# Kernel optimization log

Hardware: AMD Instinct MI355X
Metric: run time of the kernel (lower is better)

## Reference

```python
import jax, jax.numpy as jnp
import numpy as np

N = 50000   # nodes
E = 800000  # edges (avg degree 16)
D = 64      # input_nf = output_nf = hidden_nf


def lrelu(x):
    # nn.LeakyReLU(0.2)
    return jnp.where(x >= 0, x, 0.2 * x)


def setup_inputs() -> dict:
    key = jax.random.key(0)
    ks = jax.random.split(key, 12)
    def lin(k, fan_in, fan_out):
        s = 1.0 / np.sqrt(fan_in)
        return jax.random.uniform(k, (fan_in, fan_out), jnp.float32, -s, s)
    inp = {
        "h": jax.random.normal(ks[0], (N, D), jnp.float32),
        "coord": jax.random.normal(ks[1], (N, 3), jnp.float32),
        "edge_index": jax.random.randint(ks[2], (2, E), 0, N, jnp.int32),
        # edge_mlp: Linear(2D+1, D) -> lrelu -> Linear(D, D) -> lrelu
        "w1e": lin(ks[3], 2 * D + 1, D), "b1e": jnp.zeros((D,), jnp.float32),
        "w2e": lin(ks[4], D, D),         "b2e": jnp.zeros((D,), jnp.float32),
        # node_mlp: Linear(2D, D) -> lrelu -> Linear(D, D)
        "w1n": lin(ks[5], 2 * D, D),     "b1n": jnp.zeros((D,), jnp.float32),
        "w2n": lin(ks[6], D, D),         "b2n": jnp.zeros((D,), jnp.float32),
    }
    return inp


def reference(h, coord, edge_index, w1e, b1e, w2e, b2e, w1n, b1n, w2n, b2n):
    row, col = edge_index[0], edge_index[1]
    # coord2radial
    coord_diff = coord[row] - coord[col]                    # [E, 3]
    radial = jnp.sum(coord_diff ** 2, axis=1, keepdims=True)  # [E, 1]
    # edge_model: concat(h[row], h[col], radial) -> MLP
    e_in = jnp.concatenate([h[row], h[col], radial], axis=1)  # [E, 2D+1]
    e = lrelu(e_in @ w1e + b1e)
    edge_feat = lrelu(e @ w2e + b2e)                        # [E, D]
    # node_model: unsorted_segment_sum over row, then MLP, residual
    agg = jax.ops.segment_sum(edge_feat, row, num_segments=N)  # [N, D]
    n_in = jnp.concatenate([h, agg], axis=1)                # [N, 2D]
    out = lrelu(n_in @ w1n + b1n) @ w2n + b2n               # [N, D]
    h_out = h + out                                         # residual=True
    # coords_weight == 0.0 -> coord passes through unchanged
    return (h_out, coord, edge_feat)
```

## Files before the change

kernel.cpp:

```cpp
#include <hip/hip_runtime.h>

#define NN 50000
#define NE 800000
#define D 64
#define SCAN_B 1024
#define NB ((NN + SCAN_B - 1) / SCAN_B)
#define TILES 5
#define EPB (64 * TILES)

typedef __attribute__((ext_vector_type(8))) short bf16x8;
typedef __attribute__((ext_vector_type(4))) float f32x4;
typedef __attribute__((ext_vector_type(4))) unsigned int u32x4;

__device__ __forceinline__ float lrelu(float x) { return x >= 0.0f ? x : 0.2f * x; }

__device__ __forceinline__ unsigned short f2bf(float f) {
    unsigned int x = __float_as_uint(f);
    unsigned int r = (x + 0x7fffu + ((x >> 16) & 1u)) >> 16;
    return (unsigned short)r;
}

__device__ __forceinline__ void wave_lds_fence() {
    asm volatile("s_waitcnt lgkmcnt(0)" ::: "memory");
    __builtin_amdgcn_sched_barrier(0);
}

__global__ __launch_bounds__(256) void prep_count(const float* __restrict__ h,
                                                  unsigned short* __restrict__ hb,
                                                  const int* __restrict__ ei,
                                                  int* __restrict__ counts,
                                                  const float* __restrict__ w1e,
                                                  const float* __restrict__ w2e,
                                                  const float* __restrict__ w1n,
                                                  const float* __restrict__ w2n,
                                                  unsigned short* __restrict__ w1t,
                                                  unsigned short* __restrict__ w2t,
                                                  unsigned short* __restrict__ w1nt,
                                                  unsigned short* __restrict__ w2nt)
{
    int i = blockIdx.x * 256 + threadIdx.x;
    float4 v = ((const float4*)h)[i];
    ushort4 o;
    o.x = f2bf(v.x); o.y = f2bf(v.y); o.z = f2bf(v.z); o.w = f2bf(v.w);
    ((ushort4*)hb)[i] = o;
    atomicAdd(&counts[ei[i]], 1);
    if (i < 8192) {
        int j = i >> 7, k = i & 127;
        w1t[i] = f2bf(w1e[k * 64 + j]);
    } else if (i < 12288) {
        int t2 = i - 8192;
        int j = t2 >> 6, k = t2 & 63;
        w2t[t2] = f2bf(w2e[k * 64 + j]);
    } else if (i < 20480) {
        int t3 = i - 12288;
        int j = t3 >> 7, k = t3 & 127;
        w1nt[t3] = f2bf(w1n[k * 64 + j]);
    } else if (i < 24576) {
        int t4 = i - 20480;
        int j = t4 >> 6, k = t4 & 63;
        w2nt[t4] = f2bf(w2n[k * 64 + j]);
    }
}

__global__ __launch_bounds__(SCAN_B) void scan_block_kernel(const int* __restrict__ counts,
                                                            int* __restrict__ offs,
                                                            int* __restrict__ bsums)
{
    int i = blockIdx.x * SCAN_B + threadIdx.x;
    int v = (i < NN) ? counts[i] : 0;
    int lane = threadIdx.x & 63;
    int wid = threadIdx.x >> 6;
    int x = v;
#pragma unroll
    for (int d = 1; d < 64; d <<= 1) {
        int y = __shfl_up(x, d);
        if (lane >= d) x += y;
    }
    __shared__ int wsum[16];
    if (lane == 63) wsum[wid] = x;
    __syncthreads();
    if (wid == 0) {
        int s = (lane < 16) ? wsum[lane] : 0;
#pragma unroll
        for (int d = 1; d < 16; d <<= 1) {
            int y = __shfl_up(s, d);
            if (lane >= d) s += y;
        }
        if (lane < 16) wsum[lane] = s;
    }
    __syncthreads();
    int woff = (wid == 0) ? 0 : wsum[wid - 1];
    int excl = woff + x - v;
    if (i < NN) offs[i] = excl;
    if (threadIdx.x == 0) bsums[blockIdx.x] = wsum[15];
}

__global__ void scan_top_kernel(int* __restrict__ bsums)
{
    if (threadIdx.x == 0 && blockIdx.x == 0) {
        int run = 0;
        for (int b = 0; b < NB; b++) { int t = bsums[b]; bsums[b] = run; run += t; }
    }
}

__global__ __launch_bounds__(SCAN_B) void add_back_kernel(int* __restrict__ offs,
                                                          const int* __restrict__ bsums,
                                                          int* __restrict__ cursor)
{
    int i = blockIdx.x * SCAN_B + threadIdx.x;
    if (i < NN) {
        int o = offs[i] + bsums[blockIdx.x];
        offs[i] = o;
        cursor[i] = o;
    }
}

__global__ __launch_bounds__(256) void scatter_kernel(const int* __restrict__ ei,
                                                      int* __restrict__ cursor,
                                                      int* __restrict__ csr,
                                                      int* __restrict__ rowpos,
                                                      int* __restrict__ colv)
{
    int e = blockIdx.x * 256 + threadIdx.x;
    if (e < NE) {
        int r = ei[e];
        int pos = atomicAdd(&cursor[r], 1);
        csr[pos] = e;
        rowpos[pos] = r;
        colv[pos] = ei[NE + e];
    }
}

__global__ __launch_bounds__(256) void egnn_edge_mfma(
    const unsigned short* __restrict__ hb, const float* __restrict__ coord,
    const int* __restrict__ csr, const int* __restrict__ rowpos,
    const int* __restrict__ colv,
    const unsigned short* __restrict__ w1t, const float* __restrict__ b1e,
    const float* __restrict__ w1e,
    const unsigned short* __restrict__ w2t, const float* __restrict__ b2e,
    float* __restrict__ edge_feat, float* __restrict__ agg)
{
    __shared__ unsigned short W1[64 * 128];
    __shared__ unsigned short W2[64 * 64];
    __shared__ unsigned short Mb[4][16 * 64];
    __shared__ float Ob[4][16 * 64];

    const int t = threadIdx.x;
    const int orig = blockIdx.x;
    const int xcd = orig & 7, idx8 = orig >> 3;
    const int blk = (xcd < 4 ? xcd * 313 : 4 * 313 + (xcd - 4) * 312) + idx8;

    const int lane = t & 63, wv = t >> 6;
    const int lo = lane & 15, hi = lane >> 4;

    for (int c = t; c < 1024; c += 256) {
        int j = c >> 4, ci = c & 15;
        uint4 v = *(const uint4*)(w1t + j * 128 + ci * 8);
        *(uint4*)((char*)W1 + ((j * 256 + ci * 16) ^ ((j & 7) << 4))) = v;
    }
    for (int c = t; c < 512; c += 256) {
        int j = c >> 3, ci = c & 7;
        uint4 v = *(const uint4*)(w2t + j * 64 + ci * 8);
        *(uint4*)((char*)W2 + ((j * 128 + ci * 16) ^ ((j & 7) << 4))) = v;
    }
    float bj1[4], wl1[4], bj2[4];
#pragma unroll
    for (int ct = 0; ct < 4; ct++) {
        bj1[ct] = b1e[ct * 16 + lo];
        wl1[ct] = w1e[128 * 64 + ct * 16 + lo];
        bj2[ct] = b2e[ct * 16 + lo];
    }
    __syncthreads();

    char* w1b = (char*)W1;
    char* w2b = (char*)W2;
    char* mb = (char*)Mb[wv];
    char* ob = (char*)Ob[wv];

    const int pbase = blk * EPB + wv * (16 * TILES);

    int e5[TILES], row5[TILES], col5[TILES];
    float rad5[TILES];
#pragma unroll
    for (int tl = 0; tl < TILES; tl++) {
        int p = pbase + tl * 16 + lo;
        e5[tl] = csr[p];
        row5[tl] = rowpos[p];
        col5[tl] = colv[p];
    }
#pragma unroll
    for (int tl = 0; tl < TILES; tl++) {
        float dx = coord[row5[tl] * 3 + 0] - coord[col5[tl] * 3 + 0];
        float dy = coord[row5[tl] * 3 + 1] - coord[col5[tl] * 3 + 1];
        float dz = coord[row5[tl] * 3 + 2] - coord[col5[tl] * 3 + 2];
        rad5[tl] = dx * dx + dy * dy + dz * dz;
    }

    uint4 aR0, aR1, aC0, aC1, nR0, nR1, nC0, nC1;
    aR0 = *(const uint4*)(hb + (size_t)row5[0] * 64 + hi * 8);
    aR1 = *(const uint4*)(hb + (size_t)row5[0] * 64 + 32 + hi * 8);
    aC0 = *(const uint4*)(hb + (size_t)col5[0] * 64 + hi * 8);
    aC1 = *(const uint4*)(hb + (size_t)col5[0] * 64 + 32 + hi * 8);

#pragma unroll
    for (int tl = 0; tl < TILES; tl++) {
        if (tl + 1 < TILES) {
            nR0 = *(const uint4*)(hb + (size_t)row5[tl + 1] * 64 + hi * 8);
            nR1 = *(const uint4*)(hb + (size_t)row5[tl + 1] * 64 + 32 + hi * 8);
            nC0 = *(const uint4*)(hb + (size_t)col5[tl + 1] * 64 + hi * 8);
            nC1 = *(const uint4*)(hb + (size_t)col5[tl + 1] * 64 + 32 + hi * 8);
        }

        float radr[4];
#pragma unroll
        for (int r = 0; r < 4; r++) radr[r] = __shfl(rad5[tl], hi * 4 + r);
        f32x4 acc[4];
#pragma unroll
        for (int ct = 0; ct < 4; ct++)
#pragma unroll
            for (int r = 0; r < 4; r++) acc[ct][r] = fmaf(radr[r], wl1[ct], bj1[ct]);

        bf16x8 af0 = *reinterpret_cast<bf16x8*>(&aR0);
        bf16x8 af1 = *reinterpret_cast<bf16x8*>(&aR1);
        bf16x8 af2 = *reinterpret_cast<bf16x8*>(&aC0);
        bf16x8 af3 = *reinterpret_cast<bf16x8*>(&aC1);
#pragma unroll
        for (int kc = 0; kc < 4; kc++) {
            bf16x8 a = (kc == 0) ? af0 : (kc == 1) ? af1 : (kc == 2) ? af2 : af3;
#pragma unroll
            for (int ct = 0; ct < 4; ct++) {
                bf16x8 b = *(bf16x8*)(w1b + (((ct * 16 + lo) * 256 + kc * 64 + hi * 16) ^ ((lo & 7) << 4)));
                acc[ct] = __builtin_amdgcn_mfma_f32_16x16x32_bf16(a, b, acc[ct], 0, 0, 0);
            }
        }

#pragma unroll
        for (int ct = 0; ct < 4; ct++)
#pragma unroll
            for (int r = 0; r < 4; r++) {
                int row = hi * 4 + r;
                *(unsigned short*)(mb + ((row * 128 + (ct * 16 + lo) * 2) ^ ((row & 7) << 4))) =
                    f2bf(lrelu(acc[ct][r]));
            }
        wave_lds_fence();

        f32x4 acc2[4];
#pragma unroll
        for (int ct = 0; ct < 4; ct++)
#pragma unroll
            for (int r = 0; r < 4; r++) acc2[ct][r] = bj2[ct];
#pragma unroll
        for (int kc = 0; kc < 2; kc++) {
            bf16x8 a2 = *(bf16x8*)(mb + ((lo * 128 + kc * 64 + hi * 16) ^ ((lo & 7) << 4)));
#pragma unroll
            for (int ct = 0; ct < 4; ct++) {
                bf16x8 b = *(bf16x8*)(w2b + (((ct * 16 + lo) * 128 + kc * 64 + hi * 16) ^ ((lo & 7) << 4)));
                acc2[ct] = __builtin_amdgcn_mfma_f32_16x16x32_bf16(a2, b, acc2[ct], 0, 0, 0);
            }
        }

#pragma unroll
        for (int ct = 0; ct < 4; ct++)
#pragma unroll
            for (int r = 0; r < 4; r++) {
                int row = hi * 4 + r;
                *(float*)(ob + ((row * 256 + (ct * 16 + lo) * 4) ^ ((row & 7) << 4))) =
                    lrelu(acc2[ct][r]);
            }
        wave_lds_fence();

#pragma unroll
        for (int o = 0; o < 4; o++) {
            int ridx = o * 4 + hi;
            int ee = __shfl(e5[tl], ridx);
            u32x4 v = *(u32x4*)(ob + ((ridx * 256 + lo * 16) ^ ((ridx & 7) << 4)));
            __builtin_nontemporal_store(v, (u32x4*)(edge_feat + (size_t)ee * 64 + lo * 4));
        }
        {
            int cur = __shfl(row5[tl], 0);
            float s = *(float*)(ob + ((lane * 4) ^ 0));
#pragma unroll
            for (int ii = 1; ii < 16; ii++) {
                int r = __shfl(row5[tl], ii);
                float v = *(float*)(ob + ((ii * 256 + lane * 4) ^ ((ii & 7) << 4)));
                if (r != cur) {
                    atomicAdd(&agg[(size_t)cur * 64 + lane], s);
                    s = v; cur = r;
                } else {
                    s += v;
                }
            }
            atomicAdd(&agg[(size_t)cur * 64 + lane], s);
        }

        aR0 = nR0; aR1 = nR1; aC0 = nC0; aC1 = nC1;
    }
}

__global__ __launch_bounds__(256) void agg_node_mfma(
    const unsigned short* __restrict__ hb, const float* __restrict__ h,
    const float* __restrict__ coord, const float* __restrict__ agg,
    const unsigned short* __restrict__ w1nt, const float* __restrict__ b1n,
    const unsigned short* __restrict__ w2nt, const float* __restrict__ b2n,
    float* __restrict__ h_out, float* __restrict__ coord_out)
{
    __shared__ unsigned short Alds[64 * 128];
    __shared__ unsigned short Mlds[64 * 64];

    const int t = threadIdx.x, blk = blockIdx.x;
    const int lane = t & 63, wv = t >> 6;
    const int lo = lane & 15, hi = lane >> 4;
    const int nb = blk * 64;
    char* abase = (char*)Alds;
    char* mbase = (char*)Mlds;

    bf16x8 b1f[4], b2f[2];
#pragma unroll
    for (int kc = 0; kc < 4; kc++)
        b1f[kc] = *(const bf16x8*)(w1nt + (wv * 16 + lo) * 128 + kc * 32 + hi * 8);
#pragma unroll
    for (int kc = 0; kc < 2; kc++)
        b2f[kc] = *(const bf16x8*)(w2nt + (wv * 16 + lo) * 64 + kc * 32 + hi * 8);
    const float bj1 = b1n[wv * 16 + lo];
    const float bj2 = b2n[wv * 16 + lo];

    {
        int row = t >> 2, seg = t & 3;
        int n = min(nb + row, NN - 1);
        const uint4* src = (const uint4*)(hb + (size_t)n * 64 + seg * 16);
        int base = row * 256 + seg * 32;
        int swr = (row & 7) << 4;
        uint4 v0 = src[0], v1 = src[1];
        *(uint4*)(abase + (base ^ swr)) = v0;
        *(uint4*)(abase + ((base + 16) ^ swr)) = v1;
    }
    {
        int row = t >> 2, seg = t & 3;
        int n = min(nb + row, NN - 1);
        const float4* asrc = (const float4*)(agg + (size_t)n * 64 + seg * 16);
        float4 a0 = asrc[0], a1 = asrc[1], a2 = asrc[2], a3 = asrc[3];
        unsigned int u0 = f2bf(a0.x) | ((unsigned)f2bf(a0.y) << 16);
        unsigned int u1 = f2bf(a0.z) | ((unsigned)f2bf(a0.w) << 16);
        unsigned int u2 = f2bf(a1.x) | ((unsigned)f2bf(a1.y) << 16);
        unsigned int u3 = f2bf(a1.z) | ((unsigned)f2bf(a1.w) << 16);
        unsigned int u4 = f2bf(a2.x) | ((unsigned)f2bf(a2.y) << 16);
        unsigned int u5 = f2bf(a2.z) | ((unsigned)f2bf(a2.w) << 16);
        unsigned int u6 = f2bf(a3.x) | ((unsigned)f2bf(a3.y) << 16);
        unsigned int u7 = f2bf(a3.z) | ((unsigned)f2bf(a3.w) << 16);
        int base = row * 256 + 128 + seg * 32;
        int swr = (row & 7) << 4;
        *(uint4*)(abase + (base ^ swr)) = make_uint4(u0, u1, u2, u3);
        *(uint4*)(abase + ((base + 16) ^ swr)) = make_uint4(u4, u5, u6, u7);
    }
    __syncthreads();

    f32x4 acc[4];
#pragma unroll
    for (int rt = 0; rt < 4; rt++) {
#pragma unroll
        for (int r = 0; r < 4; r++) acc[rt][r] = bj1;
    }
#pragma unroll
    for (int kc = 0; kc < 4; kc++) {
#pragma unroll
        for (int rt = 0; rt < 4; rt++) {
            int row = rt * 16 + lo;
            bf16x8 a = *(bf16x8*)(abase + ((row * 256 + kc * 64 + hi * 16) ^ ((row & 7) << 4)));
            acc[rt] = __builtin_amdgcn_mfma_f32_16x16x32_bf16(a, b1f[kc], acc[rt], 0, 0, 0);
        }
    }
#pragma unroll
    for (int rt = 0; rt < 4; rt++) {
#pragma unroll
        for (int r = 0; r < 4; r++) {
            int row = rt * 16 + hi * 4 + r;
            *(unsigned short*)(mbase + ((row * 128 + (wv * 16 + lo) * 2) ^ ((row & 7) << 4))) =
                f2bf(lrelu(acc[rt][r]));
        }
    }
    __syncthreads();

    f32x4 acc2[4];
#pragma unroll
    for (int rt = 0; rt < 4; rt++) {
#pragma unroll
        for (int r = 0; r < 4; r++) acc2[rt][r] = bj2;
    }
#pragma unroll
    for (int kc = 0; kc < 2; kc++) {
#pragma unroll
        for (int rt = 0; rt < 4; rt++) {
            int row = rt * 16 + lo;
            bf16x8 a = *(bf16x8*)(mbase + ((row * 128 + kc * 64 + hi * 16) ^ ((row & 7) << 4)));
            acc2[rt] = __builtin_amdgcn_mfma_f32_16x16x32_bf16(a, b2f[kc], acc2[rt], 0, 0, 0);
        }
    }
#pragma unroll
    for (int rt = 0; rt < 4; rt++) {
#pragma unroll
        for (int r = 0; r < 4; r++) {
            int row = rt * 16 + hi * 4 + r;
            int n = nb + row;
            if (n < NN) {
                int c = wv * 16 + lo;
                float v = h[(size_t)n * 64 + c] + acc2[rt][r];
                __builtin_nontemporal_store(v, h_out + (size_t)n * 64 + c);
            }
        }
    }

    if (t < 192) {
        int idx = nb * 3 + t;
        if (idx < NN * 3) coord_out[idx] = coord[idx];
    }
}

extern "C" void kernel_launch(void* const* d_in, const int* in_sizes, int n_in,
                              void* d_out, int out_size, void* d_ws, size_t ws_size,
                              hipStream_t stream)
{
    const float* h     = (const float*)d_in[0];
    const float* coord = (const float*)d_in[1];
    const int*   ei    = (const int*)d_in[2];
    const float* w1e   = (const float*)d_in[3];
    const float* b1e   = (const float*)d_in[4];
    const float* w2e   = (const float*)d_in[5];
    const float* b2e   = (const float*)d_in[6];
    const float* w1n   = (const float*)d_in[7];
    const float* b1n   = (const float*)d_in[8];
    const float* w2n   = (const float*)d_in[9];
    const float* b2n   = (const float*)d_in[10];

    float* out       = (float*)d_out;
    float* h_out     = out;
    float* coord_out = out + (size_t)NN * D;
    float* edge_feat = coord_out + (size_t)NN * 3;

    char* ws = (char*)d_ws;
    unsigned short* hb   = (unsigned short*)ws;  ws += sizeof(unsigned short) * (size_t)NN * D;
    unsigned short* w1t  = (unsigned short*)ws;  ws += sizeof(unsigned short) * 64 * 128;
    unsigned short* w2t  = (unsigned short*)ws;  ws += sizeof(unsigned short) * 64 * 64;
    unsigned short* w1nt = (unsigned short*)ws;  ws += sizeof(unsigned short) * 64 * 128;
    unsigned short* w2nt = (unsigned short*)ws;  ws += sizeof(unsigned short) * 64 * 64;
    float* agg  = (float*)ws;                    ws += sizeof(float) * (size_t)NN * D;
    int* counts = (int*)ws;                      ws += sizeof(int) * NN;
    int* offs   = (int*)ws;                      ws += sizeof(int) * NN;
    int* cursor = (int*)ws;                      ws += sizeof(int) * NN;
    int* bsums  = (int*)ws;                      ws += sizeof(int) * 64;
    int* csr    = (int*)ws;                      ws += sizeof(int) * NE;
    int* rowpos = (int*)ws;                      ws += sizeof(int) * NE;
    int* colv   = (int*)ws;                      ws += sizeof(int) * NE;

    hipMemsetAsync(counts, 0, sizeof(int) * NN, stream);
    hipMemsetAsync(agg, 0, sizeof(float) * (size_t)NN * D, stream);

    prep_count<<<NE / 256, 256, 0, stream>>>(h, hb, ei, counts,
                                             w1e, w2e, w1n, w2n, w1t, w2t, w1nt, w2nt);

    scan_block_kernel<<<NB, SCAN_B, 0, stream>>>(counts, offs, bsums);
    scan_top_kernel<<<1, 64, 0, stream>>>(bsums);
    add_back_kernel<<<NB, SCAN_B, 0, stream>>>(offs, bsums, cursor);
    scatter_kernel<<<(NE + 255) / 256, 256, 0, stream>>>(ei, cursor, csr, rowpos, colv);

    egnn_edge_mfma<<<NE / EPB, 256, 0, stream>>>(
        hb, coord, csr, rowpos, colv, w1t, b1e, w1e, w2t, b2e, edge_feat, agg);

    agg_node_mfma<<<(NN + 63) / 64, 256, 0, stream>>>(
        hb, h, coord, agg, w1nt, b1n, w2nt, b2n, h_out, coord_out);
}
```

Measured before the change: 202.5 us.

## Stage edge outputs in bf16 LDS and carry segment sums across tiles

```diff
diff --git a/kernel.cpp b/kernel.cpp
--- a/kernel.cpp
+++ b/kernel.cpp
@@ -19,10 +19,8 @@
     unsigned int r = (x + 0x7fffu + ((x >> 16) & 1u)) >> 16;
     return (unsigned short)r;
 }
-
-__device__ __forceinline__ void wave_lds_fence() {
-    asm volatile("s_waitcnt lgkmcnt(0)" ::: "memory");
-    __builtin_amdgcn_sched_barrier(0);
+__device__ __forceinline__ float bf2f(unsigned short u) {
+    return __uint_as_float(((unsigned int)u) << 16);
 }
 
 __global__ __launch_bounds__(256) void prep_count(const float* __restrict__ h,
@@ -143,7 +141,7 @@
     __shared__ unsigned short W1[64 * 128];
     __shared__ unsigned short W2[64 * 64];
     __shared__ unsigned short Mb[4][16 * 64];
-    __shared__ float Ob[4][16 * 64];
+    __shared__ unsigned short Obf[4][16 * 64];
 
     const int t = threadIdx.x;
     const int orig = blockIdx.x;
@@ -175,7 +173,7 @@
     char* w1b = (char*)W1;
     char* w2b = (char*)W2;
     char* mb = (char*)Mb[wv];
-    char* ob = (char*)Ob[wv];
+    char* ob = (char*)Obf[wv];
 
     const int pbase = blk * EPB + wv * (16 * TILES);
 
@@ -201,6 +199,9 @@
     aR1 = *(const uint4*)(hb + (size_t)row5[0] * 64 + 32 + hi * 8);
     aC0 = *(const uint4*)(hb + (size_t)col5[0] * 64 + hi * 8);
     aC1 = *(const uint4*)(hb + (size_t)col5[0] * 64 + 32 + hi * 8);
+
+    int curSeg = -1;
+    float sSeg = 0.0f;
 
 #pragma unroll
     for (int tl = 0; tl < TILES; tl++) {
@@ -242,7 +243,6 @@
                 *(unsigned short*)(mb + ((row * 128 + (ct * 16 + lo) * 2) ^ ((row & 7) << 4))) =
                     f2bf(lrelu(acc[ct][r]));
             }
-        wave_lds_fence();
 
         f32x4 acc2[4];
 #pragma unroll
@@ -264,37 +264,37 @@
 #pragma unroll
             for (int r = 0; r < 4; r++) {
                 int row = hi * 4 + r;
-                *(float*)(ob + ((row * 256 + (ct * 16 + lo) * 4) ^ ((row & 7) << 4))) =
-                    lrelu(acc2[ct][r]);
-            }
-        wave_lds_fence();
+                *(unsigned short*)(ob + ((row * 128 + (ct * 16 + lo) * 2) ^ ((row & 7) << 4))) =
+                    f2bf(lrelu(acc2[ct][r]));
+            }
 
 #pragma unroll
         for (int o = 0; o < 4; o++) {
             int ridx = o * 4 + hi;
             int ee = __shfl(e5[tl], ridx);
-            u32x4 v = *(u32x4*)(ob + ((ridx * 256 + lo * 16) ^ ((ridx & 7) << 4)));
+            uint2 uv = *(uint2*)(ob + ((ridx * 128 + lo * 8) ^ ((ridx & 7) << 4)));
+            u32x4 v;
+            v.x = (uv.x & 0xffffu) << 16;
+            v.y = (uv.x & 0xffff0000u);
+            v.z = (uv.y & 0xffffu) << 16;
+            v.w = (uv.y & 0xffff0000u);
             __builtin_nontemporal_store(v, (u32x4*)(edge_feat + (size_t)ee * 64 + lo * 4));
         }
-        {
-            int cur = __shfl(row5[tl], 0);
-            float s = *(float*)(ob + ((lane * 4) ^ 0));
-#pragma unroll
-            for (int ii = 1; ii < 16; ii++) {
-                int r = __shfl(row5[tl], ii);
-                float v = *(float*)(ob + ((ii * 256 + lane * 4) ^ ((ii & 7) << 4)));
-                if (r != cur) {
-                    atomicAdd(&agg[(size_t)cur * 64 + lane], s);
-                    s = v; cur = r;
-                } else {
-                    s += v;
-                }
-            }
-            atomicAdd(&agg[(size_t)cur * 64 + lane], s);
+#pragma unroll
+        for (int ii = 0; ii < 16; ii++) {
+            int r = __shfl(row5[tl], ii);
+            float v = bf2f(*(unsigned short*)(ob + ((ii * 128 + lane * 2) ^ ((ii & 7) << 4))));
+            if (r != curSeg) {
+                if (curSeg >= 0) atomicAdd(&agg[(size_t)curSeg * 64 + lane], sSeg);
+                sSeg = v; curSeg = r;
+            } else {
+                sSeg += v;
+            }
         }
 
         aR0 = nR0; aR1 = nR1; aC0 = nC0; aC1 = nC1;
     }
+    atomicAdd(&agg[(size_t)curSeg * 64 + lane], sSeg);
 }
 
 __global__ __launch_bounds__(256) void agg_node_mfma(
```

Measured after the change: 205.8 us. No clear change (+1.6%).
